# Performance work log

Measured on AMD Instinct MI355X. Metric: run time of the kernel, lower is better.

## Reference

```python
import jax, jax.numpy as jnp
import numpy as np

D_MODEL, D_STATE, D_CONV, EXPAND = 1024, 16, 4, 2
D_INNER = EXPAND * D_MODEL            # 2048
DT_RANK = (D_MODEL + 15) // 16        # 64 (mamba 'auto')
B, L = 2, 2048
EPS = 1e-5


def setup_inputs() -> dict:
    key = jax.random.key(0)
    ks = jax.random.split(key, 12)
    s = lambda k, shape, sc=0.02: jax.random.normal(k, shape, dtype=jnp.float32) * sc
    return {
        "x": jax.random.normal(ks[0], (B, L, D_MODEL), dtype=jnp.float32),
        "ln_w": jnp.ones((D_MODEL,), jnp.float32),
        "ln_b": jnp.zeros((D_MODEL,), jnp.float32),
        "W_in": s(ks[1], (2 * D_INNER, D_MODEL)),
        "conv_w": s(ks[2], (D_INNER, D_CONV), 0.2),
        "conv_b": jnp.zeros((D_INNER,), jnp.float32),
        "W_xproj": s(ks[3], (DT_RANK + 2 * D_STATE, D_INNER)),
        "W_dt": s(ks[4], (D_INNER, DT_RANK), 0.1),
        "b_dt": jax.random.uniform(ks[5], (D_INNER,), jnp.float32, -4.0, -2.0),  # softplus(b)~dt_min
        "A_log": jnp.log(jnp.broadcast_to(jnp.arange(1, D_STATE + 1, dtype=jnp.float32), (D_INNER, D_STATE))),
        "D": jnp.ones((D_INNER,), jnp.float32),
        "W_out": s(ks[6], (D_MODEL, D_INNER)),
    }


def _mamba_forward(x, ln_w, ln_b, W_in, conv_w, conv_b, W_xproj, W_dt, b_dt, A_log, D, W_out):
    # Pre-norm LayerNorm
    mu = jnp.mean(x, axis=-1, keepdims=True)
    var = jnp.mean(jnp.square(x - mu), axis=-1, keepdims=True)
    xn = (x - mu) * jax.lax.rsqrt(var + EPS) * ln_w + ln_b

    # in_proj -> [B, L, 2*d_inner]; split into x-branch and gate z
    xz = jnp.einsum("bld,ed->ble", xn, W_in)
    u, z = jnp.split(xz, 2, axis=-1)

    # causal depthwise conv1d over L, kernel width D_CONV
    u_pad = jnp.pad(u, ((0, 0), (D_CONV - 1, 0), (0, 0)))
    uc = conv_b[None, None, :]
    for k in range(D_CONV):
        uc = uc + u_pad[:, k:k + L, :] * conv_w[:, k]
    u = jax.nn.silu(uc)  # [B, L, d_inner]

    # input-dependent dt, B, C
    dbl = jnp.einsum("bld,ed->ble", u, W_xproj)
    dt_r = dbl[..., :DT_RANK]
    Bm = dbl[..., DT_RANK:DT_RANK + D_STATE]          # [B, L, n]
    Cm = dbl[..., DT_RANK + D_STATE:]                 # [B, L, n]
    dt = jax.nn.softplus(jnp.einsum("blr,dr->bld", dt_r, W_dt) + b_dt)  # [B, L, d]

    A = -jnp.exp(A_log)  # [d, n]

    # selective scan over L; carry h: [B, d, n]
    def step(h, inp):
        dt_t, B_t, C_t, u_t = inp  # [B,d], [B,n], [B,n], [B,d]
        dA = jnp.exp(dt_t[:, :, None] * A[None])                 # [B, d, n]
        h = dA * h + (dt_t * u_t)[:, :, None] * B_t[:, None, :]  # [B, d, n]
        y_t = jnp.einsum("bdn,bn->bd", h, C_t)
        return h, y_t

    xs = (jnp.moveaxis(dt, 1, 0), jnp.moveaxis(Bm, 1, 0),
          jnp.moveaxis(Cm, 1, 0), jnp.moveaxis(u, 1, 0))
    h0 = jnp.zeros((x.shape[0], D_INNER, D_STATE), x.dtype)
    _, ys = jax.lax.scan(step, h0, xs)
    y = jnp.moveaxis(ys, 0, 1) + u * D  # [B, L, d_inner]

    y = y * jax.nn.silu(z)
    out = jnp.einsum("bld,ed->ble", y, W_out)
    return x + out


def reference(x, ln_w, ln_b, W_in, conv_w, conv_b, W_xproj, W_dt, b_dt, A_log, D, W_out):
    return _mamba_forward(x, ln_w, ln_b, W_in, conv_w, conv_b, W_xproj, W_dt, b_dt, A_log, D, W_out)
```

## Files before the change

kernel.cpp:

```cpp
#include <hip/hip_runtime.h>
#include <hip/hip_bf16.h>
#include <stdint.h>

typedef __hip_bfloat16 bf16;
typedef __attribute__((ext_vector_type(8))) short short8;
typedef __attribute__((ext_vector_type(4))) float floatx4;

#define D_MODEL 1024
#define D_STATE 16
#define D_INNER 2048
#define DT_RANK 64
#define BB 2
#define LL 2048
#define BL (BB * LL)
#define XZ_LD (2 * D_INNER)
#define DBL_LD (DT_RANK + 2 * D_STATE)
#define NCH 64
#define TCH (LL / NCH)

__device__ __forceinline__ bf16 f2b(float f) { return __float2bfloat16(f); }

__device__ __forceinline__ float fsig(float v)  { return __fdividef(1.f, 1.f + __expf(-v)); }
__device__ __forceinline__ float fsoftp(float v){ return fmaxf(v, 0.f) + __logf(1.f + __expf(-fabsf(v))); }

__device__ __forceinline__ void gload16(const void* g, void* l) {
    __builtin_amdgcn_global_load_lds(
        (const __attribute__((address_space(1))) uint32_t*)(uintptr_t)g,
        (__attribute__((address_space(3))) uint32_t*)(uintptr_t)l,
        16, 0, 0);
}

#define S0 (4096 * 1024)
#define S1 (128 * 2048)
#define S2 (2048 * 64)
#define S3 (1024 * 2048)
#define S4 (BL * DBL_LD)
#define WCVT_TOT (S0 + S1 + S2 + S3 + S4)

__global__ __launch_bounds__(256) void prep_kernel(
    const float* __restrict__ x, const float* __restrict__ w,
    const float* __restrict__ b, bf16* __restrict__ xnb,
    const float* __restrict__ Win, const float* __restrict__ Wx,
    const float* __restrict__ Wdt, const float* __restrict__ Wout,
    bf16* __restrict__ win_bf, bf16* __restrict__ wx_bf,
    bf16* __restrict__ wdt_bf, bf16* __restrict__ wout_bf,
    float* __restrict__ dbl)
{
    __shared__ float s1[256], s2[256];
    const int tid = threadIdx.x;
    if (blockIdx.x < BL) {
        const int row = blockIdx.x;
        const float* xr = x + (size_t)row * D_MODEL;
        float v[4], sum = 0.f, sq = 0.f;
#pragma unroll
        for (int i = 0; i < 4; ++i) {
            v[i] = xr[tid + 256 * i];
            sum += v[i];
            sq  += v[i] * v[i];
        }
        s1[tid] = sum; s2[tid] = sq;
        __syncthreads();
        for (int s = 128; s > 0; s >>= 1) {
            if (tid < s) { s1[tid] += s1[tid + s]; s2[tid] += s2[tid + s]; }
            __syncthreads();
        }
        const float mu  = s1[0] * (1.f / D_MODEL);
        const float var = s2[0] * (1.f / D_MODEL) - mu * mu;
        const float rs  = rsqrtf(var + 1e-5f);
#pragma unroll
        for (int i = 0; i < 4; ++i) {
            const int c = tid + 256 * i;
            xnb[(size_t)row * D_MODEL + c] = f2b((v[i] - mu) * rs * w[c] + b[c]);
        }
    } else {
        int id = (blockIdx.x - BL) * 256 + tid;
        if (id < S0) { win_bf[id] = f2b(Win[id]); return; }
        id -= S0;
        if (id < S1) { wx_bf[id] = (id < 96 * 2048) ? f2b(Wx[id]) : f2b(0.f); return; }
        id -= S1;
        if (id < S2) { wdt_bf[id] = f2b(Wdt[id]); return; }
        id -= S2;
        if (id < S3) { wout_bf[id] = f2b(Wout[id]); return; }
        id -= S3;
        dbl[id] = 0.f;
    }
}

#define GTM 128
#define GTN 128
#define GTK 32

template <int EPI>
__global__ __launch_bounds__(256) void gemm_t(
    const bf16* __restrict__ A, int lda,
    const bf16* __restrict__ B, int ldb,
    float* __restrict__ C, int ldc,
    int N, int K,
    const float* __restrict__ bias,
    bf16* __restrict__ C2)
{
    __shared__ short As[GTM * GTK];
    __shared__ short Bs[GTN * GTK];
    const int tid  = threadIdx.x;
    const int lane = tid & 63;
    const int wave = tid >> 6;
    const int wm = (wave & 1) * 64;
    const int wn = (wave >> 1) * 64;
    const int bm = blockIdx.y * GTM;
    const int bn = blockIdx.x * GTN;
    const int kbase = blockIdx.z * K;

    floatx4 acc[4][4];
#pragma unroll
    for (int i = 0; i < 4; ++i)
#pragma unroll
        for (int j = 0; j < 4; ++j) acc[i][j] = (floatx4){0.f, 0.f, 0.f, 0.f};

    const int srow = wave * 16 + (lane >> 2);
    const int scol = (lane & 3) * 8;
    const int fm = lane & 15;
    const int q  = lane >> 4;

    for (int k0 = 0; k0 < K; k0 += GTK) {
#pragma unroll
        for (int r = 0; r < 2; ++r) {
            const int m = r * 64 + srow;
            gload16(A + (size_t)(bm + m) * lda + kbase + k0 + scol,
                    As + m * GTK + scol);
            gload16(B + (size_t)(bn + m) * ldb + kbase + k0 + scol,
                    Bs + m * GTK + scol);
        }
        __syncthreads();

        short8 af[4], bfr[4];
#pragma unroll
        for (int i = 0; i < 4; ++i)
            af[i] = *(short8*)&As[(wm + i * 16 + fm) * GTK + q * 8];
#pragma unroll
        for (int j = 0; j < 4; ++j)
            bfr[j] = *(short8*)&Bs[(wn + j * 16 + fm) * GTK + q * 8];
#pragma unroll
        for (int i = 0; i < 4; ++i)
#pragma unroll
            for (int j = 0; j < 4; ++j)
                acc[i][j] = __builtin_amdgcn_mfma_f32_16x16x32_bf16(
                    af[i], bfr[j], acc[i][j], 0, 0, 0);
        __syncthreads();
    }

    const int col = lane & 15;
    const int rq  = (lane >> 4) * 4;
#pragma unroll
    for (int i = 0; i < 4; ++i) {
#pragma unroll
        for (int j = 0; j < 4; ++j) {
#pragma unroll
            for (int r = 0; r < 4; ++r) {
                const int gm = bm + wm + i * 16 + rq + r;
                const int gn = bn + wn + j * 16 + col;
                if (gn >= N) continue;
                float v = acc[i][j][r];
                if constexpr (EPI == 3) {
                    atomicAdd(&C[(size_t)gm * ldc + gn], v);
                } else if constexpr (EPI == 4) {
                    if (gn < D_INNER) C[(size_t)gm * ldc + gn] = v;
                    else C2[(size_t)gm * (size_t)D_INNER + (gn - D_INNER)] = f2b(v);
                } else {
                    C2[(size_t)gm * ldc + gn] = f2b(fsoftp(v + bias[gn]));
                }
            }
        }
    }
}

#define PNT (D_MODEL / 64)

__global__ __launch_bounds__(512, 2) void gemm256_uz(
    const bf16* __restrict__ A,
    const bf16* __restrict__ B,
    float* __restrict__ U,
    bf16* __restrict__ Z)
{
    __shared__ __attribute__((aligned(16))) short lds[65536];
    const int t    = threadIdx.x;
    const int lane = t & 63;
    const int wid  = t >> 6;
    const int wm   = wid >> 2;
    const int wn   = wid & 3;
    const int fm   = lane & 15;
    const int q    = lane >> 4;

    const int lin = (int)blockIdx.x;
    const int nid = (lin & 7) * 32 + (lin >> 3);
    const int bm  = (nid >> 4) * 256;
    const int bn  = (nid & 15) * 256;

    const int sg   = (((t & 7) ^ ((t >> 3) & 7)) << 3);
    const int ldst = t * 8;
    const short* Agp = (const short*)A + (size_t)(bm + (t >> 3)) * D_MODEL + sg;
    const short* Bgp = (const short*)B + (size_t)(bn + (t >> 3)) * D_MODEL + sg;

#define STG(g, lb) do { \
        gload16((g),                           &lds[(lb) + ldst]);        \
        gload16((g) + (size_t)64 * D_MODEL,    &lds[(lb) + 4096 + ldst]); \
    } while (0)

    const int ss0 = ((q ^ (fm & 7)) << 3);
    const int ss1 = (((4 + q) ^ (fm & 7)) << 3);
    const int aro = fm * 64;
    const int bro = ((wn & 1) * 64 + fm) * 64;

    floatx4 acc[8][4];
#pragma unroll
    for (int i = 0; i < 8; ++i)
#pragma unroll
        for (int j = 0; j < 4; ++j) acc[i][j] = (floatx4){0.f, 0.f, 0.f, 0.f};

    STG(Agp, 0);
    STG(Agp + (size_t)128 * D_MODEL, 8192);
    STG(Bgp, 32768);
    STG(Bgp + (size_t)128 * D_MODEL, 32768 + 8192);

    for (int kt = 0; kt < PNT; ++kt) {
        __syncthreads();
        const int d  = kt & 1;
        const short* Ab = &lds[d * 16384 + wm * 8192];
        const short* Bb = &lds[32768 + d * 16384 + (wn >> 1) * 8192];
        const int kn = (kt + 1) * 64;
        const int nb = (d ^ 1) * 16384;

        short8 bfr[4][2];
#pragma unroll
        for (int cf = 0; cf < 4; ++cf) {
            bfr[cf][0] = *(const short8*)(Bb + bro + cf * 1024 + ss0);
            bfr[cf][1] = *(const short8*)(Bb + bro + cf * 1024 + ss1);
        }

#pragma unroll
        for (int qd = 0; qd < 4; ++qd) {
            short8 af[2][2];
#pragma unroll
            for (int i = 0; i < 2; ++i) {
                af[i][0] = *(const short8*)(Ab + (qd * 2 + i) * 1024 + aro + ss0);
                af[i][1] = *(const short8*)(Ab + (qd * 2 + i) * 1024 + aro + ss1);
            }
            if (qd == 0 && kt < PNT - 1) {
                STG(Agp + kn,                        nb);
                STG(Agp + (size_t)128 * D_MODEL + kn, nb + 8192);
            }
            if (qd == 1 && kt < PNT - 1) {
                STG(Bgp + kn,                        32768 + nb);
                STG(Bgp + (size_t)128 * D_MODEL + kn, 32768 + nb + 8192);
            }
            __builtin_amdgcn_s_barrier();
            __builtin_amdgcn_s_setprio(1);
#pragma unroll
            for (int i = 0; i < 2; ++i)
#pragma unroll
                for (int cf = 0; cf < 4; ++cf) {
                    acc[qd * 2 + i][cf] = __builtin_amdgcn_mfma_f32_16x16x32_bf16(
                        af[i][0], bfr[cf][0], acc[qd * 2 + i][cf], 0, 0, 0);
                    acc[qd * 2 + i][cf] = __builtin_amdgcn_mfma_f32_16x16x32_bf16(
                        af[i][1], bfr[cf][1], acc[qd * 2 + i][cf], 0, 0, 0);
                }
            __builtin_amdgcn_s_setprio(0);
            if (qd < 3) __builtin_amdgcn_s_barrier();
        }
    }
#undef STG

    const int gm0 = bm + wm * 128 + q * 4;
    const int gn0 = bn + wn * 64 + fm;
    if (bn < D_INNER) {
#pragma unroll
        for (int rf = 0; rf < 8; ++rf)
#pragma unroll
            for (int cf = 0; cf < 4; ++cf)
#pragma unroll
                for (int r = 0; r < 4; ++r)
                    U[(size_t)(gm0 + rf * 16 + r) * D_INNER + gn0 + cf * 16] =
                        acc[rf][cf][r];
    } else {
#pragma unroll
        for (int rf = 0; rf < 8; ++rf)
#pragma unroll
            for (int cf = 0; cf < 4; ++cf)
#pragma unroll
                for (int r = 0; r < 4; ++r)
                    Z[(size_t)(gm0 + rf * 16 + r) * D_INNER + gn0 + cf * 16 - D_INNER] =
                        f2b(acc[rf][cf][r]);
    }
}

#define OTM 128
#define OTN 64

__global__ __launch_bounds__(256) void gemm_out(
    const bf16* __restrict__ A, int lda,
    const bf16* __restrict__ B, int ldb,
    const float* __restrict__ resid,
    float* __restrict__ C)
{
    __shared__ short As[OTM * GTK];
    __shared__ short Bs[OTN * GTK];
    const int tid  = threadIdx.x;
    const int lane = tid & 63;
    const int wave = tid >> 6;
    const int wm = (wave & 1) * 64;
    const int wn = (wave >> 1) * 32;
    const int bm = blockIdx.y * OTM;
    const int bn = blockIdx.x * OTN;

    floatx4 acc[4][2];
#pragma unroll
    for (int i = 0; i < 4; ++i)
#pragma unroll
        for (int j = 0; j < 2; ++j) acc[i][j] = (floatx4){0.f, 0.f, 0.f, 0.f};

    const int srow = wave * 16 + (lane >> 2);
    const int scol = (lane & 3) * 8;
    const int fm = lane & 15;
    const int q  = lane >> 4;

    for (int k0 = 0; k0 < D_INNER; k0 += GTK) {
        gload16(A + (size_t)(bm + srow) * lda + k0 + scol,
                As + srow * GTK + scol);
        gload16(A + (size_t)(bm + 64 + srow) * lda + k0 + scol,
                As + (64 + srow) * GTK + scol);
        gload16(B + (size_t)(bn + srow) * ldb + k0 + scol,
                Bs + srow * GTK + scol);
        __syncthreads();

        short8 af[4], bfr[2];
#pragma unroll
        for (int i = 0; i < 4; ++i)
            af[i] = *(short8*)&As[(wm + i * 16 + fm) * GTK + q * 8];
#pragma unroll
        for (int j = 0; j < 2; ++j)
            bfr[j] = *(short8*)&Bs[(wn + j * 16 + fm) * GTK + q * 8];
#pragma unroll
        for (int i = 0; i < 4; ++i)
#pragma unroll
            for (int j = 0; j < 2; ++j)
                acc[i][j] = __builtin_amdgcn_mfma_f32_16x16x32_bf16(
                    af[i], bfr[j], acc[i][j], 0, 0, 0);
        __syncthreads();
    }

    const int col = lane & 15;
    const int rq  = (lane >> 4) * 4;
#pragma unroll
    for (int i = 0; i < 4; ++i) {
#pragma unroll
        for (int j = 0; j < 2; ++j) {
#pragma unroll
            for (int r = 0; r < 4; ++r) {
                const int gm = bm + wm + i * 16 + rq + r;
                const int gn = bn + wn + j * 16 + col;
                C[(size_t)gm * D_MODEL + gn] =
                    acc[i][j][r] + resid[(size_t)gm * D_MODEL + gn];
            }
        }
    }
}

__global__ __launch_bounds__(256) void conv_par3(
    const float* __restrict__ uraw, const float* __restrict__ cw,
    const float* __restrict__ cb, bf16* __restrict__ ucb)
{
    const int id = blockIdx.x * 256 + threadIdx.x;
    const int d = id & (D_INNER - 1);
    const int t = (id >> 11) & (LL - 1);
    float acc = cb[d];
#pragma unroll
    for (int k = 0; k < 4; ++k) {
        const int tt = t - 3 + k;
        if (tt >= 0)
            acc += uraw[(size_t)id + (size_t)(k - 3) * D_INNER] * cw[d * 4 + k];
    }
    ucb[id] = f2b(acc * fsig(acc));
}

__global__ __launch_bounds__(256) void cvt_dtr(
    const float* __restrict__ dbl, bf16* __restrict__ dtr_bf)
{
    const int id = blockIdx.x * 256 + threadIdx.x;
    const int m = id >> 6, r = id & 63;
    dtr_bf[id] = f2b(dbl[(size_t)m * DBL_LD + r]);
}

__global__ __launch_bounds__(256) void scan_p1(
    const bf16* __restrict__ uc, const bf16* __restrict__ dtb,
    const float* __restrict__ dbl, const float* __restrict__ A_log,
    float* __restrict__ Psum, float* __restrict__ Hloc)
{
    const int blk = blockIdx.x;
    const int d = (blk & 7) * 256 + threadIdx.x;
    const int c = (blk >> 3) & (NCH - 1);
    const int b = blk >> 9;
    float A[D_STATE], h[D_STATE];
    bool lin = true;
#pragma unroll
    for (int n = 0; n < D_STATE; ++n) {
        A[n] = -__expf(A_log[d * D_STATE + n]);
        lin = lin && (fabsf(A[n] + (float)(n + 1)) < 1e-3f);
        h[n] = 0.f;
    }
    const size_t row0 = (size_t)b * LL + c * TCH;
    const bf16* dtp = dtb + row0 * D_INNER + d;
    const bf16* up  = uc  + row0 * D_INNER + d;
    const float* Bp = dbl + row0 * DBL_LD + DT_RANK;
    float S = 0.f;
    if (lin) {
        for (int t = 0; t < TCH; ++t) {
            const float dtv = (float)dtp[(size_t)t * D_INNER];
            const float uv  = (float)up[(size_t)t * D_INNER];
            const float du  = dtv * uv;
            S += dtv;
            const float e1 = __expf(-dtv);
            float dA = 1.f;
#pragma unroll
            for (int n = 0; n < D_STATE; ++n) {
                dA *= e1;
                h[n] = dA * h[n] + du * Bp[(size_t)t * DBL_LD + n];
            }
        }
    } else {
        for (int t = 0; t < TCH; ++t) {
            const float dtv = (float)dtp[(size_t)t * D_INNER];
            const float uv  = (float)up[(size_t)t * D_INNER];
            const float du  = dtv * uv;
            S += dtv;
#pragma unroll
            for (int n = 0; n < D_STATE; ++n)
                h[n] = __expf(dtv * A[n]) * h[n] + du * Bp[(size_t)t * DBL_LD + n];
        }
    }
    const size_t o = (((size_t)b * NCH + c) * D_INNER + d) * D_STATE;
    if (lin) {
        const float E1 = __expf(-S);
        float P = 1.f;
#pragma unroll
        for (int n = 0; n < D_STATE; ++n) {
            P *= E1;
            Psum[o + n] = P;
            Hloc[o + n] = h[n];
        }
    } else {
#pragma unroll
        for (int n = 0; n < D_STATE; ++n) {
            Psum[o + n] = __expf(S * A[n]);
            Hloc[o + n] = h[n];
        }
    }
}

__global__ __launch_bounds__(256) void scan_p2(
    float* __restrict__ Psum, const float* __restrict__ Hloc)
{
    const int id = blockIdx.x * 256 + threadIdx.x;
    const int dn = id & (D_INNER * D_STATE - 1);
    const int b  = id >> 15;
    float h = 0.f;
    for (int c = 0; c < NCH; ++c) {
        const size_t o = ((size_t)(b * NCH + c) * D_INNER * D_STATE) + dn;
        const float P  = Psum[o];
        const float hl = Hloc[o];
        Psum[o] = h;
        h = P * h + hl;
    }
}

__global__ __launch_bounds__(256) void scan_p3b(
    bf16* __restrict__ ucy, const bf16* __restrict__ dtb,
    const float* __restrict__ dbl, const float* __restrict__ A_log,
    const float* __restrict__ Dw, const float* __restrict__ Hin,
    const bf16* __restrict__ zbf)
{
    const int blk = blockIdx.x;
    const int d = (blk & 7) * 256 + threadIdx.x;
    const int c = (blk >> 3) & (NCH - 1);
    const int b = blk >> 9;
    float A[D_STATE], h[D_STATE];
    const size_t o = (((size_t)b * NCH + c) * D_INNER + d) * D_STATE;
    bool lin = true;
#pragma unroll
    for (int n = 0; n < D_STATE; ++n) {
        A[n] = -__expf(A_log[d * D_STATE + n]);
        lin = lin && (fabsf(A[n] + (float)(n + 1)) < 1e-3f);
        h[n] = Hin[o + n];
    }
    const float Dd = Dw[d];
    const size_t row0 = (size_t)b * LL + c * TCH;
    const bf16* dtp = dtb + row0 * D_INNER + d;
    bf16*       uyp = ucy + row0 * D_INNER + d;
    const float* BCp = dbl + row0 * DBL_LD;
    const bf16* zp   = zbf + row0 * D_INNER + d;
    if (lin) {
        for (int t = 0; t < TCH; ++t) {
            const float dtv = (float)dtp[(size_t)t * D_INNER];
            const float uv  = (float)uyp[(size_t)t * D_INNER];
            const float du  = dtv * uv;
            float acc = uv * Dd;
            const float* Brow = BCp + (size_t)t * DBL_LD + DT_RANK;
            const float* Crow = Brow + D_STATE;
            const float e1 = __expf(-dtv);
            float dA = 1.f;
#pragma unroll
            for (int n = 0; n < D_STATE; ++n) {
                dA *= e1;
                h[n] = dA * h[n] + du * Brow[n];
                acc += h[n] * Crow[n];
            }
            const float zv = (float)zp[(size_t)t * D_INNER];
            uyp[(size_t)t * D_INNER] = f2b(acc * zv * fsig(zv));
        }
    } else {
        for (int t = 0; t < TCH; ++t) {
            const float dtv = (float)dtp[(size_t)t * D_INNER];
            const float uv  = (float)uyp[(size_t)t * D_INNER];
            const float du  = dtv * uv;
            float acc = uv * Dd;
            const float* Brow = BCp + (size_t)t * DBL_LD + DT_RANK;
            const float* Crow = Brow + D_STATE;
#pragma unroll
            for (int n = 0; n < D_STATE; ++n) {
                h[n] = __expf(dtv * A[n]) * h[n] + du * Brow[n];
                acc += h[n] * Crow[n];
            }
            const float zv = (float)zp[(size_t)t * D_INNER];
            uyp[(size_t)t * D_INNER] = f2b(acc * zv * fsig(zv));
        }
    }
}

#define BM 128
#define BN 128
#define BK 8

__global__ __launch_bounds__(256) void ln_kernel(
    const float* __restrict__ x, const float* __restrict__ w,
    const float* __restrict__ b, float* __restrict__ xnf)
{
    __shared__ float s1[256], s2[256];
    const int row = blockIdx.x;
    const int tid = threadIdx.x;
    const float* xr = x + (size_t)row * D_MODEL;
    float v[4], sum = 0.f, sq = 0.f;
#pragma unroll
    for (int i = 0; i < 4; ++i) {
        v[i] = xr[tid + 256 * i];
        sum += v[i];
        sq  += v[i] * v[i];
    }
    s1[tid] = sum; s2[tid] = sq;
    __syncthreads();
    for (int s = 128; s > 0; s >>= 1) {
        if (tid < s) { s1[tid] += s1[tid + s]; s2[tid] += s2[tid + s]; }
        __syncthreads();
    }
    const float mu  = s1[0] * (1.f / D_MODEL);
    const float var = s2[0] * (1.f / D_MODEL) - mu * mu;
    const float rs  = rsqrtf(var + 1e-5f);
#pragma unroll
    for (int i = 0; i < 4; ++i) {
        const int c = tid + 256 * i;
        xnf[(size_t)row * D_MODEL + c] = (v[i] - mu) * rs * w[c] + b[c];
    }
}

__global__ __launch_bounds__(256) void gemm_bt(
    const float* __restrict__ A, int lda,
    const float* __restrict__ Bw,
    float* __restrict__ C, int ldc,
    int M, int N, int K, int epi,
    const float* __restrict__ bias,
    const float* __restrict__ resid)
{
    __shared__ float As[BK][BM + 1];
    __shared__ float Bs[BK][BN + 1];
    const int tx = threadIdx.x, ty = threadIdx.y;
    const int tid = ty * 16 + tx;
    const int bm = blockIdx.y * BM, bn = blockIdx.x * BN;
    float acc[8][8];
#pragma unroll
    for (int i = 0; i < 8; ++i)
#pragma unroll
        for (int j = 0; j < 8; ++j) acc[i][j] = 0.f;
    for (int k0 = 0; k0 < K; k0 += BK) {
#pragma unroll
        for (int i = tid; i < BM * BK; i += 256) {
            const int m = i / BK, kk = i % BK;
            As[kk][m] = A[(size_t)(bm + m) * lda + (k0 + kk)];
        }
#pragma unroll
        for (int i = tid; i < BN * BK; i += 256) {
            const int n = i / BK, kk = i % BK;
            const int gn = bn + n;
            Bs[kk][n] = (gn < N) ? Bw[(size_t)gn * K + (k0 + kk)] : 0.f;
        }
        __syncthreads();
#pragma unroll
        for (int kk = 0; kk < BK; ++kk) {
            float av[8], bv[8];
#pragma unroll
            for (int i = 0; i < 8; ++i) av[i] = As[kk][ty * 8 + i];
#pragma unroll
            for (int j = 0; j < 8; ++j) bv[j] = Bs[kk][tx * 8 + j];
#pragma unroll
            for (int i = 0; i < 8; ++i)
#pragma unroll
                for (int j = 0; j < 8; ++j) acc[i][j] += av[i] * bv[j];
        }
        __syncthreads();
    }
#pragma unroll
    for (int i = 0; i < 8; ++i) {
        const int gm = bm + ty * 8 + i;
#pragma unroll
        for (int j = 0; j < 8; ++j) {
            const int gn = bn + tx * 8 + j;
            if (gn >= N) continue;
            float v = acc[i][j];
            if (epi == 1) {
                v += bias[gn];
                v = fmaxf(v, 0.f) + log1pf(expf(-fabsf(v)));
            } else if (epi == 2) {
                v += resid[(size_t)gm * ldc + gn];
            }
            C[(size_t)gm * ldc + gn] = v;
        }
    }
}

__global__ __launch_bounds__(256) void conv_silu_kernel(
    float* __restrict__ xz, const float* __restrict__ cw,
    const float* __restrict__ cb)
{
    const int idx = blockIdx.x * 256 + threadIdx.x;
    const int b = idx >> 11, d = idx & (D_INNER - 1);
    const float w0 = cw[d * 4 + 0], w1 = cw[d * 4 + 1];
    const float w2 = cw[d * 4 + 2], w3 = cw[d * 4 + 3];
    const float bias = cb[d];
    float* u = xz + (size_t)b * LL * XZ_LD + d;
    float x0 = 0.f, x1 = 0.f, x2 = 0.f;
    for (int t = 0; t < LL; ++t) {
        const float x3 = u[(size_t)t * XZ_LD];
        const float c = bias + x0 * w0 + x1 * w1 + x2 * w2 + x3 * w3;
        u[(size_t)t * XZ_LD] = c / (1.f + expf(-c));
        x0 = x1; x1 = x2; x2 = x3;
    }
}

__global__ __launch_bounds__(256) void scan_kernel(
    float* __restrict__ xz, const float* __restrict__ dtb,
    const float* __restrict__ dbl,
    const float* __restrict__ A_log, const float* __restrict__ Dw)
{
    const int idx = blockIdx.x * 256 + threadIdx.x;
    const int b = idx >> 11, d = idx & (D_INNER - 1);
    float A[D_STATE], h[D_STATE];
#pragma unroll
    for (int n = 0; n < D_STATE; ++n) {
        A[n] = -expf(A_log[d * D_STATE + n]);
        h[n] = 0.f;
    }
    const float Dd = Dw[d];
    const float* dtp  = dtb + (size_t)b * LL * D_INNER + d;
    float*       up   = xz  + (size_t)b * LL * XZ_LD + d;
    const float* dblp = dbl + (size_t)b * LL * DBL_LD;
    for (int t = 0; t < LL; ++t) {
        const float dtv = dtp[(size_t)t * D_INNER];
        const float uv  = up[(size_t)t * XZ_LD];
        const float zv  = up[(size_t)t * XZ_LD + D_INNER];
        const float* Brow = dblp + (size_t)t * DBL_LD + DT_RANK;
        const float* Crow = Brow + D_STATE;
        const float du = dtv * uv;
        float acc = uv * Dd;
#pragma unroll
        for (int n = 0; n < D_STATE; ++n) {
            const float dA = expf(dtv * A[n]);
            h[n] = dA * h[n] + du * Brow[n];
            acc += h[n] * Crow[n];
        }
        const float sz = zv / (1.f + expf(-zv));
        up[(size_t)t * XZ_LD] = acc * sz;
    }
}

extern "C" void kernel_launch(void* const* d_in, const int* in_sizes, int n_in,
                              void* d_out, int out_size, void* d_ws, size_t ws_size,
                              hipStream_t stream)
{
    const float* x       = (const float*)d_in[0];
    const float* ln_w    = (const float*)d_in[1];
    const float* ln_b    = (const float*)d_in[2];
    const float* W_in    = (const float*)d_in[3];
    const float* conv_w  = (const float*)d_in[4];
    const float* conv_b  = (const float*)d_in[5];
    const float* W_xproj = (const float*)d_in[6];
    const float* W_dt    = (const float*)d_in[7];
    const float* b_dt    = (const float*)d_in[8];
    const float* A_log   = (const float*)d_in[9];
    const float* Dw      = (const float*)d_in[10];
    const float* W_out   = (const float*)d_in[11];
    float* out = (float*)d_out;

    float* wsf     = (float*)d_ws;
    bf16*  dtb_bf  = (bf16*)wsf;
    float* uraw    = wsf + 4194304;
    bf16*  zbf     = (bf16*)(wsf + 12582912);
    float* Psum    = wsf + 16777216;
    float* Hloc    = wsf + 20971520;
    float* dbl     = wsf + 25165824;
    bf16*  ucy     = (bf16*)(wsf + 25559040);
    bf16*  xn_bf   = (bf16*)(wsf + 29753344);
    bf16*  win_bf  = (bf16*)(wsf + 31850496);
    bf16*  wx_bf   = (bf16*)(wsf + 33947648);
    bf16*  wdt_bf  = (bf16*)(wsf + 34078720);
    bf16*  wout_bf = (bf16*)(wsf + 34144256);
    bf16*  dtr_bf  = (bf16*)(wsf + 35192832);
    const size_t need_big = (size_t)35323904 * sizeof(float);

    if (ws_size >= need_big) {
        prep_kernel<<<BL + WCVT_TOT / 256, 256, 0, stream>>>(
            x, ln_w, ln_b, xn_bf,
            W_in, W_xproj, W_dt, W_out, win_bf, wx_bf, wdt_bf, wout_bf, dbl);
        gemm256_uz<<<dim3(256), 512, 0, stream>>>(xn_bf, win_bf, uraw, zbf);
        conv_par3<<<(size_t)BL * D_INNER / 256, 256, 0, stream>>>(
            uraw, conv_w, conv_b, ucy);
        gemm_t<3><<<dim3(1, BL / GTM, 8), 256, 0, stream>>>(
            ucy, D_INNER, wx_bf, D_INNER, dbl, DBL_LD,
            DBL_LD, D_INNER / 8, nullptr, nullptr);
        cvt_dtr<<<BL * DT_RANK / 256, 256, 0, stream>>>(dbl, dtr_bf);
        gemm_t<5><<<dim3(D_INNER / GTN, BL / GTM, 1), 256, 0, stream>>>(
            dtr_bf, DT_RANK, wdt_bf, DT_RANK, nullptr, D_INNER,
            D_INNER, DT_RANK, b_dt, dtb_bf);
        scan_p1<<<BB * NCH * 8, 256, 0, stream>>>(
            ucy, dtb_bf, dbl, A_log, Psum, Hloc);
        scan_p2<<<BB * D_INNER * D_STATE / 256, 256, 0, stream>>>(Psum, Hloc);
        scan_p3b<<<BB * NCH * 8, 256, 0, stream>>>(
            ucy, dtb_bf, dbl, A_log, Dw, Psum, zbf);
        gemm_out<<<dim3(D_MODEL / OTN, BL / OTM), 256, 0, stream>>>(
            ucy, D_INNER, wout_bf, D_INNER, x, out);
    } else {
        float* fdtb = wsf;
        float* fxn  = fdtb;
        float* fxz  = fdtb + (size_t)BL * D_INNER;
        float* fdbl = fxz + (size_t)BL * XZ_LD;
        ln_kernel<<<BL, 256, 0, stream>>>(x, ln_w, ln_b, fxn);
        dim3 blk(16, 16);
        gemm_bt<<<dim3(XZ_LD / BN, BL / BM), blk, 0, stream>>>(
            fxn, D_MODEL, W_in, fxz, XZ_LD, BL, XZ_LD, D_MODEL, 0, nullptr, nullptr);
        conv_silu_kernel<<<(BB * D_INNER) / 256, 256, 0, stream>>>(fxz, conv_w, conv_b);
        gemm_bt<<<dim3(1, BL / BM), blk, 0, stream>>>(
            fxz, XZ_LD, W_xproj, fdbl, DBL_LD, BL, DBL_LD, D_INNER, 0, nullptr, nullptr);
        gemm_bt<<<dim3(D_INNER / BN, BL / BM), blk, 0, stream>>>(
            fdbl, DBL_LD, W_dt, fdtb, D_INNER, BL, D_INNER, DT_RANK, 1, b_dt, nullptr);
        scan_kernel<<<(BB * D_INNER) / 256, 256, 0, stream>>>(fxz, fdtb, fdbl, A_log, Dw);
        gemm_bt<<<dim3(D_MODEL / BN, BL / BM), blk, 0, stream>>>(
            fxz, XZ_LD, W_out, out, D_MODEL, BL, D_MODEL, D_INNER, 2, nullptr, x);
    }
}
```

Measured before the change: 322.2 us.

## Double-buffer out-projection GEMM with swizzled LDS and rewrite conv as sliding window

The out-projection GEMM is replaced by a 512-thread, 128x128-tile kernel. It uses K=64 stages, double-buffered XOR-swizzled shared memory, prefetch of the next tile interleaved with MFMA work, setprio hints, and a remapped block order for L2 locality. The depthwise conv now has each thread handle 4 channels over a 16-step time chunk with a sliding register window and vectorized loads and stores, instead of one thread per output reading 4 inputs. Together these aim to cut LDS stalls, global re-reads and launch granularity, at the cost of more LDS per block and more complex indexing.

```diff
diff --git a/kernel.cpp b/kernel.cpp
--- a/kernel.cpp
+++ b/kernel.cpp
@@ -4,6 +4,7 @@
 
 typedef __hip_bfloat16 bf16;
 typedef __attribute__((ext_vector_type(8))) short short8;
+typedef __attribute__((ext_vector_type(4))) short short4v;
 typedef __attribute__((ext_vector_type(4))) float floatx4;
 
 #define D_MODEL 1024
@@ -292,24 +293,41 @@
     }
 }
 
-#define OTM 128
-#define OTN 64
-
-__global__ __launch_bounds__(256) void gemm_out(
-    const bf16* __restrict__ A, int lda,
-    const bf16* __restrict__ B, int ldb,
+#define ONT (D_INNER / 64)
+
+__global__ __launch_bounds__(512, 2) void gemm_out8(
+    const bf16* __restrict__ A,
+    const bf16* __restrict__ B,
     const float* __restrict__ resid,
     float* __restrict__ C)
 {
-    __shared__ short As[OTM * GTK];
-    __shared__ short Bs[OTN * GTK];
-    const int tid  = threadIdx.x;
-    const int lane = tid & 63;
-    const int wave = tid >> 6;
-    const int wm = (wave & 1) * 64;
-    const int wn = (wave >> 1) * 32;
-    const int bm = blockIdx.y * OTM;
-    const int bn = blockIdx.x * OTN;
+    __shared__ __attribute__((aligned(16))) short lds[32768];
+    const int t    = threadIdx.x;
+    const int lane = t & 63;
+    const int wid  = t >> 6;
+    const int wm   = wid >> 2;
+    const int wn   = wid & 3;
+    const int fm   = lane & 15;
+    const int q    = lane >> 4;
+
+    const int lin = (int)blockIdx.x;
+    const int nid = (lin & 7) * 32 + (lin >> 3);
+    const int bm  = (nid >> 3) * 128;
+    const int bn  = (nid & 7) * 128;
+
+    const int sg   = (((t & 7) ^ ((t >> 3) & 7)) << 3);
+    const int ldst = t * 8;
+    const short* Agp = (const short*)A + (size_t)(bm + (t >> 3)) * D_INNER + sg;
+    const short* Bgp = (const short*)B + (size_t)(bn + (t >> 3)) * D_INNER + sg;
+
+#define OSTG(g, lb) do { \
+        gload16((g),                        &lds[(lb) + ldst]);        \
+        gload16((g) + (size_t)64 * D_INNER, &lds[(lb) + 4096 + ldst]); \
+    } while (0)
+
+    const int ss0 = ((q ^ (fm & 7)) << 3);
+    const int ss1 = (((4 + q) ^ (fm & 7)) << 3);
+    const int fro = fm * 64;
 
     floatx4 acc[4][2];
 #pragma unroll
@@ -317,68 +335,109 @@
 #pragma unroll
         for (int j = 0; j < 2; ++j) acc[i][j] = (floatx4){0.f, 0.f, 0.f, 0.f};
 
-    const int srow = wave * 16 + (lane >> 2);
-    const int scol = (lane & 3) * 8;
-    const int fm = lane & 15;
-    const int q  = lane >> 4;
-
-    for (int k0 = 0; k0 < D_INNER; k0 += GTK) {
-        gload16(A + (size_t)(bm + srow) * lda + k0 + scol,
-                As + srow * GTK + scol);
-        gload16(A + (size_t)(bm + 64 + srow) * lda + k0 + scol,
-                As + (64 + srow) * GTK + scol);
-        gload16(B + (size_t)(bn + srow) * ldb + k0 + scol,
-                Bs + srow * GTK + scol);
+    OSTG(Agp, 0);
+    OSTG(Bgp, 16384);
+
+    for (int kt = 0; kt < ONT; ++kt) {
         __syncthreads();
-
-        short8 af[4], bfr[2];
-#pragma unroll
-        for (int i = 0; i < 4; ++i)
-            af[i] = *(short8*)&As[(wm + i * 16 + fm) * GTK + q * 8];
-#pragma unroll
-        for (int j = 0; j < 2; ++j)
-            bfr[j] = *(short8*)&Bs[(wn + j * 16 + fm) * GTK + q * 8];
-#pragma unroll
-        for (int i = 0; i < 4; ++i)
-#pragma unroll
-            for (int j = 0; j < 2; ++j)
-                acc[i][j] = __builtin_amdgcn_mfma_f32_16x16x32_bf16(
-                    af[i], bfr[j], acc[i][j], 0, 0, 0);
-        __syncthreads();
-    }
-
-    const int col = lane & 15;
-    const int rq  = (lane >> 4) * 4;
-#pragma unroll
-    for (int i = 0; i < 4; ++i) {
-#pragma unroll
-        for (int j = 0; j < 2; ++j) {
+        const int d  = kt & 1;
+        const short* Ab = &lds[d * 8192 + wm * 4096];
+        const short* Bb = &lds[16384 + d * 8192 + wn * 2048];
+        const int kn = (kt + 1) * 64;
+        const int nb = (d ^ 1) * 8192;
+
+        short8 bfr[2][2];
+#pragma unroll
+        for (int cf = 0; cf < 2; ++cf) {
+            bfr[cf][0] = *(const short8*)(Bb + cf * 1024 + fro + ss0);
+            bfr[cf][1] = *(const short8*)(Bb + cf * 1024 + fro + ss1);
+        }
+
+#pragma unroll
+        for (int qd = 0; qd < 2; ++qd) {
+            short8 af[2][2];
+#pragma unroll
+            for (int i = 0; i < 2; ++i) {
+                af[i][0] = *(const short8*)(Ab + (qd * 2 + i) * 1024 + fro + ss0);
+                af[i][1] = *(const short8*)(Ab + (qd * 2 + i) * 1024 + fro + ss1);
+            }
+            if (qd == 0 && kt < ONT - 1) OSTG(Agp + kn, nb);
+            if (qd == 1 && kt < ONT - 1) OSTG(Bgp + kn, 16384 + nb);
+            __builtin_amdgcn_s_barrier();
+            __builtin_amdgcn_s_setprio(1);
+#pragma unroll
+            for (int i = 0; i < 2; ++i)
+#pragma unroll
+                for (int cf = 0; cf < 2; ++cf) {
+                    acc[qd * 2 + i][cf] = __builtin_amdgcn_mfma_f32_16x16x32_bf16(
+                        af[i][0], bfr[cf][0], acc[qd * 2 + i][cf], 0, 0, 0);
+                    acc[qd * 2 + i][cf] = __builtin_amdgcn_mfma_f32_16x16x32_bf16(
+                        af[i][1], bfr[cf][1], acc[qd * 2 + i][cf], 0, 0, 0);
+                }
+            __builtin_amdgcn_s_setprio(0);
+            if (qd == 0) __builtin_amdgcn_s_barrier();
+        }
+    }
+#undef OSTG
+
+    const int gm0 = bm + wm * 64 + q * 4;
+    const int gn0 = bn + wn * 32 + fm;
+#pragma unroll
+    for (int i = 0; i < 4; ++i)
+#pragma unroll
+        for (int cf = 0; cf < 2; ++cf)
 #pragma unroll
             for (int r = 0; r < 4; ++r) {
-                const int gm = bm + wm + i * 16 + rq + r;
-                const int gn = bn + wn + j * 16 + col;
-                C[(size_t)gm * D_MODEL + gn] =
-                    acc[i][j][r] + resid[(size_t)gm * D_MODEL + gn];
-            }
-        }
-    }
-}
-
-__global__ __launch_bounds__(256) void conv_par3(
+                const size_t idx = (size_t)(gm0 + i * 16 + r) * D_MODEL + gn0 + cf * 16;
+                C[idx] = acc[i][cf][r] + resid[idx];
+            }
+}
+
+#define CCH 128
+#define CTC (LL / CCH)
+
+__global__ __launch_bounds__(256) void conv_v2(
     const float* __restrict__ uraw, const float* __restrict__ cw,
     const float* __restrict__ cb, bf16* __restrict__ ucb)
 {
-    const int id = blockIdx.x * 256 + threadIdx.x;
-    const int d = id & (D_INNER - 1);
-    const int t = (id >> 11) & (LL - 1);
-    float acc = cb[d];
-#pragma unroll
-    for (int k = 0; k < 4; ++k) {
-        const int tt = t - 3 + k;
-        if (tt >= 0)
-            acc += uraw[(size_t)id + (size_t)(k - 3) * D_INNER] * cw[d * 4 + k];
-    }
-    ucb[id] = f2b(acc * fsig(acc));
+    const int blk = blockIdx.x;
+    const int c  = blk & (CCH - 1);
+    const int dg = (blk >> 7) & 1;
+    const int b  = blk >> 8;
+    const int d4 = dg * 1024 + threadIdx.x * 4;
+    float w0[4], w1[4], w2[4], w3[4], bias[4];
+#pragma unroll
+    for (int j = 0; j < 4; ++j) {
+        bias[j] = cb[d4 + j];
+        w0[j] = cw[(d4 + j) * 4 + 0];
+        w1[j] = cw[(d4 + j) * 4 + 1];
+        w2[j] = cw[(d4 + j) * 4 + 2];
+        w3[j] = cw[(d4 + j) * 4 + 3];
+    }
+    const size_t base = ((size_t)b * LL + (size_t)c * CTC) * D_INNER + d4;
+    floatx4 x0 = {0.f, 0.f, 0.f, 0.f}, x1 = x0, x2 = x0;
+    if (c > 0) {
+        x0 = *(const floatx4*)(uraw + base - 3 * (size_t)D_INNER);
+        x1 = *(const floatx4*)(uraw + base - 2 * (size_t)D_INNER);
+        x2 = *(const floatx4*)(uraw + base - 1 * (size_t)D_INNER);
+    }
+#pragma unroll
+    for (int tt = 0; tt < CTC; ++tt) {
+        const floatx4 x3 = *(const floatx4*)(uraw + base + (size_t)tt * D_INNER);
+        short4v o;
+#pragma unroll
+        for (int j = 0; j < 4; ++j) {
+            float a = bias[j] + x0[j] * w0[j] + x1[j] * w1[j]
+                              + x2[j] * w2[j] + x3[j] * w3[j];
+            a = a * fsig(a);
+            bf16 h = f2b(a);
+            unsigned short us;
+            __builtin_memcpy(&us, &h, 2);
+            o[j] = (short)us;
+        }
+        *(short4v*)(ucb + base + (size_t)tt * D_INNER) = o;
+        x0 = x1; x1 = x2; x2 = x3;
+    }
 }
 
 __global__ __launch_bounds__(256) void cvt_dtr(
@@ -727,8 +786,7 @@
             x, ln_w, ln_b, xn_bf,
             W_in, W_xproj, W_dt, W_out, win_bf, wx_bf, wdt_bf, wout_bf, dbl);
         gemm256_uz<<<dim3(256), 512, 0, stream>>>(xn_bf, win_bf, uraw, zbf);
-        conv_par3<<<(size_t)BL * D_INNER / 256, 256, 0, stream>>>(
-            uraw, conv_w, conv_b, ucy);
+        conv_v2<<<BB * 2 * CCH, 256, 0, stream>>>(uraw, conv_w, conv_b, ucy);
         gemm_t<3><<<dim3(1, BL / GTM, 8), 256, 0, stream>>>(
             ucy, D_INNER, wx_bf, D_INNER, dbl, DBL_LD,
             DBL_LD, D_INNER / 8, nullptr, nullptr);
@@ -741,8 +799,7 @@
         scan_p2<<<BB * D_INNER * D_STATE / 256, 256, 0, stream>>>(Psum, Hloc);
         scan_p3b<<<BB * NCH * 8, 256, 0, stream>>>(
             ucy, dtb_bf, dbl, A_log, Dw, Psum, zbf);
-        gemm_out<<<dim3(D_MODEL / OTN, BL / OTM), 256, 0, stream>>>(
-            ucy, D_INNER, wout_bf, D_INNER, x, out);
+        gemm_out8<<<dim3(256), 512, 0, stream>>>(ucy, wout_bf, x, out);
     } else {
         float* fdtb = wsf;
         float* fxn  = fdtb;
```

New measurement: 285.6 us. -11.4%, faster.
